# Kernel optimization log

Hardware: AMD Instinct MI355X
Metric: run time of the kernel (lower is better)

The kernel has to match this reference:

```python
import jax, jax.numpy as jnp
import numpy as np

EPS = 1e-5

def _conv(x, w, pad):
    return jax.lax.conv_general_dilated(
        x, w, window_strides=(1, 1), padding=((pad, pad), (pad, pad)),
        dimension_numbers=('NCHW', 'OIHW', 'NCHW'))

def _dyn_branch(x, w, d):
    # x: [N,C,H,W]; w: [N,9,H,W] softmax weights; d: dilation.
    # Equivalent to unfold(k=3, dilation=d, padding=d) + bmm with w,
    # done as 9 shifted zero-padded slices (row-major kernel order).
    N, C, H, W = x.shape
    xp = jnp.pad(x, ((0, 0), (0, 0), (d, d), (d, d)))
    out = jnp.zeros_like(x)
    k = 0
    for dy in (-d, 0, d):
        for dx in (-d, 0, d):
            patch = xp[:, :, d + dy:d + dy + H, d + dx:d + dx + W]
            out = out + patch * w[:, k:k + 1]
            k += 1
    return out

def setup_inputs() -> dict:
    key = jax.random.key(0)
    k1, k2, k3 = jax.random.split(key, 3)
    C = 256
    x = jax.random.normal(k1, (2, C, 96, 96), dtype=jnp.float32)
    W_cat = jax.random.normal(k2, (45, C, 3, 3), dtype=jnp.float32) * 0.05
    W_scale = jax.random.normal(k3, (C, 6 * C, 1, 1), dtype=jnp.float32) * 0.05
    gamma = jnp.ones((C,), dtype=jnp.float32)
    beta = jnp.zeros((C,), dtype=jnp.float32)
    return {"x": x, "W_cat": W_cat, "W_scale": W_scale, "gamma": gamma, "beta": beta}

def reference(x, W_cat, W_scale, gamma, beta):
    guidance = _conv(x, W_cat, pad=1)  # [N,45,H,W]
    outs = [x]
    for i, d in enumerate((1, 6, 12, 24, 36)):
        w = jax.nn.softmax(guidance[:, 9 * i:9 * (i + 1)], axis=1)  # [N,9,H,W]
        outs.append(_dyn_branch(x, w, d))
    cat = jnp.concatenate(outs, axis=1)  # [N, 6C, H, W]
    y = _conv(cat, W_scale, pad=0)       # [N, C, H, W]
    # BatchNorm2d in training mode (batch statistics, biased variance)
    mean = jnp.mean(y, axis=(0, 2, 3), keepdims=True)
    var = jnp.var(y, axis=(0, 2, 3), keepdims=True)
    y = (y - mean) * jax.lax.rsqrt(var + EPS)
    return y * gamma[None, :, None, None] + beta[None, :, None, None]
```

## Files before the change

### kernel.cpp

```cpp
#include <hip/hip_runtime.h>

typedef __bf16 bf16x8 __attribute__((ext_vector_type(8)));
typedef float f32x4 __attribute__((ext_vector_type(4)));

#define HW 9216
#define ZSLAB 9216
#define XTILE 32768

__device__ __forceinline__ unsigned short f2bf(float f) {
  unsigned u = __float_as_uint(f);
  unsigned r = (u + 0x7FFFu + ((u >> 16) & 1u)) >> 16;
  return (unsigned short)r;
}
__device__ __forceinline__ float bf2f(unsigned short h) {
  return __uint_as_float(((unsigned)h) << 16);
}

__device__ __forceinline__ void async16(const unsigned short* g, unsigned short* l) {
  __builtin_amdgcn_global_load_lds(
      (const __attribute__((address_space(1))) unsigned int*)g,
      (__attribute__((address_space(3))) unsigned int*)l, 16, 0, 0);
}

template <int O>
__device__ __forceinline__ void tapfma(float* y, uint4 lo, uint4 hi, uint4 wv) {
  const unsigned short* lu = (const unsigned short*)&lo;
  const unsigned short* hu = (const unsigned short*)&hi;
  const unsigned short* wu = (const unsigned short*)&wv;
#pragma unroll
  for (int j = 0; j < 8; ++j) {
    unsigned short zz = (O + j < 8) ? lu[O + j] : hu[O + j - 8];
    y[j] += bf2f(wu[j]) * bf2f(zz);
  }
}

__device__ __forceinline__ uint4 gload(const unsigned short* __restrict__ z,
                                       bool v, unsigned idx, unsigned guard) {
  return *(const uint4*)(z + (v ? idx : guard));
}

template <int B, int D>
__device__ __forceinline__ void branchU(float* y, const unsigned short* __restrict__ z,
                                        unsigned slab, unsigned guard,
                                        const unsigned short* __restrict__ gb,
                                        int h, int w0) {
  const bool cmv = ((unsigned)(w0 - ((D == 1 || D == 6) ? 8 : (D == 12 ? 16 : (D == 24 ? 24 : 40)))) <= 88u);
  const bool cm2v = ((unsigned)(w0 - ((D == 12) ? 8 : 32)) <= 88u);
  const bool cpv = ((unsigned)(w0 + ((D == 1 || D == 6) ? 8 : (D == 12 ? 16 : (D == 24 ? 24 : 40)))) <= 88u);
  const bool cp2v = ((unsigned)(w0 + ((D == 12) ? 8 : 32)) <= 88u);

#pragma unroll
  for (int r = 0; r < 3; ++r) {
    int hh = h + (r - 1) * D;
    bool rv = ((unsigned)hh < 96u);
    unsigned rb = slab + (unsigned)(hh * 96);
    const int K0 = (B - 1) * 9 + r * 3;
    uint4 wv0 = *(const uint4*)(gb + (size_t)((K0 + 0) * 2) * HW);
    uint4 wv1 = *(const uint4*)(gb + (size_t)((K0 + 1) * 2) * HW);
    uint4 wv2 = *(const uint4*)(gb + (size_t)((K0 + 2) * 2) * HW);
    if constexpr (D == 1 || D == 6) {
      uint4 Wm = gload(z, rv && cmv, rb + (unsigned)(w0 - 8), guard);
      uint4 W0 = gload(z, rv, rb + (unsigned)w0, guard);
      uint4 Wp = gload(z, rv && cpv, rb + (unsigned)(w0 + 8), guard);
      if constexpr (D == 1) {
        tapfma<7>(y, Wm, W0, wv0);
        tapfma<0>(y, W0, W0, wv1);
        tapfma<1>(y, W0, Wp, wv2);
      } else {
        tapfma<2>(y, Wm, W0, wv0);
        tapfma<0>(y, W0, W0, wv1);
        tapfma<6>(y, W0, Wp, wv2);
      }
    } else if constexpr (D == 24) {
      uint4 Wm = gload(z, rv && cmv, rb + (unsigned)(w0 - 24), guard);
      uint4 W0 = gload(z, rv, rb + (unsigned)w0, guard);
      uint4 Wp = gload(z, rv && cpv, rb + (unsigned)(w0 + 24), guard);
      tapfma<0>(y, Wm, Wm, wv0);
      tapfma<0>(y, W0, W0, wv1);
      tapfma<0>(y, Wp, Wp, wv2);
    } else {
      constexpr int co = (D == 12) ? 16 : 40;
      constexpr int ci = (D == 12) ? 8 : 32;
      uint4 Wa = gload(z, rv && cmv, rb + (unsigned)(w0 - co), guard);
      uint4 Wb = gload(z, rv && cm2v, rb + (unsigned)(w0 - ci), guard);
      uint4 W0 = gload(z, rv, rb + (unsigned)w0, guard);
      uint4 Wc = gload(z, rv && cp2v, rb + (unsigned)(w0 + ci), guard);
      uint4 Wd = gload(z, rv && cpv, rb + (unsigned)(w0 + co), guard);
      tapfma<4>(y, Wa, Wb, wv0);
      tapfma<0>(y, W0, W0, wv1);
      tapfma<4>(y, Wc, Wd, wv2);
    }
  }
}

__global__ __launch_bounds__(256) void init_all(const float* __restrict__ x,
                                                const float* __restrict__ Ws,
                                                const float* __restrict__ Wc,
                                                unsigned short* __restrict__ xb,
                                                unsigned short* __restrict__ Wsb,
                                                unsigned short* __restrict__ Wcb) {
  __shared__ float tile[64][65];
  int id = blockIdx.x;
  int t = threadIdx.x;
  if (id < 1152) {
    int bx = id % 144, by = (id / 144) % 4, n = id / 576;
    int p0 = bx * 64, ci0 = by * 64;
    int cl = t & 63, q = t >> 6;
#pragma unroll
    for (int i = 0; i < 16; ++i) {
      int cir = q + i * 4;
      tile[cir][cl] = x[((size_t)(n * 256 + ci0 + cir)) * HW + p0 + cl];
    }
    __syncthreads();
    int R = n * HW + p0 + cl;
    int Rt = R >> 7, Rl = R & 127;
#pragma unroll
    for (int i = 0; i < 2; ++i) {
      int cloc = q * 2 + i;
      unsigned rr[4];
#pragma unroll
      for (int jj = 0; jj < 4; ++jj) {
        unsigned short a = f2bf(tile[cloc * 8 + jj * 2][cl]);
        unsigned short b = f2bf(tile[cloc * 8 + jj * 2 + 1][cl]);
        rr[jj] = (unsigned)a | ((unsigned)b << 16);
      }
      *(uint4*)(xb + (size_t)Rt * XTILE + (by * 8 + cloc) * 1024 + Rl * 8) =
          make_uint4(rr[0], rr[1], rr[2], rr[3]);
    }
  } else {
    int u = (id - 1152) * 256 + t;
    if (u < 393216) {
      int r = u >> 8, k = u & 255;
      Wsb[(size_t)(r >> 7) * XTILE + (k >> 3) * 1024 + (r & 127) * 8 + (k & 7)] =
          f2bf(Ws[(size_t)(r & 255) * 1536 + (r >> 8) * 256 + k]);
    } else {
      int v = u - 393216;
      if (v < 110592) {
        int co = v / 2304, rr = v % 2304;
        int j = rr >> 8, ci = rr & 255;
        Wcb[v] = (co < 45) ? f2bf(Wc[(size_t)co * 2304 + ci * 9 + j]) : (unsigned short)0;
      }
    }
  }
}

__global__ __launch_bounds__(256) void gemms(const unsigned short* __restrict__ xb,
                                             const unsigned short* __restrict__ Wsb,
                                             const unsigned short* __restrict__ Wcb,
                                             unsigned short* __restrict__ z,
                                             unsigned short* __restrict__ gsmb) {
  __shared__ unsigned short smem[16384];
  int id = blockIdx.x;
  int t = threadIdx.x;
  int wid = t >> 6, lane = t & 63;
  int q = lane >> 4, ln = lane & 15;

  if (id < 288) {
    unsigned short* As = smem;
    unsigned short* Bs = smem + 4096;
    int m0 = id * 64;
    int mm = t >> 2, kq = t & 3;
    int m = m0 + mm;
    int img = m / HW, p = m % HW;
    int h = p / 96, w = p % 96;
    int mbase = img * HW;
    int nn = t >> 2;
    f32x4 acc[3] = {};
    uint4 aA0, aA1, aB0, aB1;

    {
      int hh = h - 1, ww = w - 1;
      bool valid = ((unsigned)hh < 96u) & ((unsigned)ww < 96u);
      int R = mbase + hh * 96 + ww;
      const unsigned short* pa =
          xb + (long)(R >> 7) * XTILE + kq * 1024 + (R & 127) * 8;
      aA0 = valid ? *(const uint4*)pa : make_uint4(0, 0, 0, 0);
      aA1 = valid ? *(const uint4*)(pa + 4096) : make_uint4(0, 0, 0, 0);
      if (t < 192) {
        const unsigned short* pb = Wcb + (size_t)nn * 2304 + kq * 8;
        aB0 = *(const uint4*)pb;
        aB1 = *(const uint4*)(pb + 32);
      }
    }

    for (int s = 0; s < 36; ++s) {
      ((uint4*)As)[kq * 64 + mm] = aA0;
      ((uint4*)As)[(kq + 4) * 64 + mm] = aA1;
      if (t < 192) {
        ((uint4*)Bs)[kq * 48 + nn] = aB0;
        ((uint4*)Bs)[(kq + 4) * 48 + nn] = aB1;
      }
      __syncthreads();
      if (s + 1 < 36) {
        int s1 = s + 1;
        int j = s1 >> 2;
        int hh = h + j / 3 - 1, ww = w + j % 3 - 1;
        bool valid = ((unsigned)hh < 96u) & ((unsigned)ww < 96u);
        int R = mbase + hh * 96 + ww;
        const unsigned short* pa = xb + (long)(R >> 7) * XTILE +
                                   ((s1 & 3) * 8 + kq) * 1024 + (R & 127) * 8;
        aA0 = valid ? *(const uint4*)pa : make_uint4(0, 0, 0, 0);
        aA1 = valid ? *(const uint4*)(pa + 4096) : make_uint4(0, 0, 0, 0);
        if (t < 192) {
          const unsigned short* pb = Wcb + (size_t)nn * 2304 + s1 * 64 + kq * 8;
          aB0 = *(const uint4*)pb;
          aB1 = *(const uint4*)(pb + 32);
        }
      }
#pragma unroll
      for (int kk = 0; kk < 2; ++kk) {
        bf16x8 a = ((const bf16x8*)As)[(kk * 4 + q) * 64 + wid * 16 + ln];
#pragma unroll
        for (int fn = 0; fn < 3; ++fn) {
          bf16x8 b = ((const bf16x8*)Bs)[(kk * 4 + q) * 48 + fn * 16 + ln];
          acc[fn] = __builtin_amdgcn_mfma_f32_16x16x32_bf16(a, b, acc[fn], 0, 0, 0);
        }
      }
      __syncthreads();
    }

    float* LDSf = (float*)smem;
#pragma unroll
    for (int fn = 0; fn < 3; ++fn)
#pragma unroll
      for (int r = 0; r < 4; ++r)
        LDSf[(wid * 16 + q * 4 + r) * 49 + fn * 16 + ln] = acc[fn][r];
    __syncthreads();
    if (t < 64) {
      const float* row = LDSf + t * 49;
      int mg = m0 + t;
      int img2 = mg / HW, p2 = mg - img2 * HW;
      for (int grp = 0; grp < 5; ++grp) {
        float v[9], mx = -1e30f;
#pragma unroll
        for (int k = 0; k < 9; ++k) { v[k] = row[grp * 9 + k]; mx = fmaxf(mx, v[k]); }
        float sum = 0.f;
#pragma unroll
        for (int k = 0; k < 9; ++k) { v[k] = __expf(v[k] - mx); sum += v[k]; }
        float inv = 1.f / sum;
#pragma unroll
        for (int k = 0; k < 9; ++k) {
          int col = grp * 9 + k;
          gsmb[((size_t)(col * 2 + img2)) * HW + p2] = f2bf(v[k] * inv);
        }
      }
    }
  } else {
    int zid = id - 288;
    int mt = zid % 144, ct = zid / 144;
    int m0 = mt * 128, c0 = ct * 128;
    int wm = (wid >> 1) * 64, wn = (wid & 1) * 64;
    bool isB = wid >= 2;
    const unsigned short* gsrc =
        (isB ? Wsb + (size_t)ct * XTILE : xb + (size_t)mt * XTILE) + lane * 8;
    unsigned short* lb = smem + (isB ? 8192 : 0);
    int ow = (wid & 1) * 4;
    f32x4 acc[4][4] = {};

#pragma unroll
    for (int kq = 0; kq < 4; ++kq)
      async16(gsrc + (ow + kq) * 512, lb + (ow + kq) * 512);
    __syncthreads();

    for (int s = 0; s < 8; ++s) {
      int cur = s & 1, nxt = cur ^ 1;
      if (s < 7) {
#pragma unroll
        for (int kq = 0; kq < 4; ++kq)
          async16(gsrc + (s + 1) * 4096 + (ow + kq) * 512,
                  lb + nxt * 4096 + (ow + kq) * 512);
      }
      const unsigned short* Asc = smem + cur * 4096;
      const unsigned short* Bsc = smem + 8192 + cur * 4096;
      bf16x8 a[4], b[4];
#pragma unroll
      for (int f = 0; f < 4; ++f) {
        a[f] = ((const bf16x8*)Asc)[q * 128 + wm + f * 16 + ln];
        b[f] = ((const bf16x8*)Bsc)[q * 128 + wn + f * 16 + ln];
      }
#pragma unroll
      for (int fm = 0; fm < 4; ++fm)
#pragma unroll
        for (int fn = 0; fn < 4; ++fn)
          acc[fm][fn] = __builtin_amdgcn_mfma_f32_16x16x32_bf16(a[fm], b[fn], acc[fm][fn], 0, 0, 0);
      __syncthreads();
    }

    int sl = c0 >> 8, cb = c0 & 255;
    int img = m0 / HW;
    int pbase = m0 - img * HW;
#pragma unroll
    for (int fm = 0; fm < 4; ++fm) {
      int p = pbase + wm + fm * 16 + q * 4;
#pragma unroll
      for (int fn = 0; fn < 4; ++fn) {
        int ch = cb + wn + fn * 16 + ln;
        size_t slab = ((size_t)(sl * 256 + ch) * 2 + img) * ZSLAB;
        unsigned lo = (unsigned)f2bf(acc[fm][fn][0]) | ((unsigned)f2bf(acc[fm][fn][1]) << 16);
        unsigned hi = (unsigned)f2bf(acc[fm][fn][2]) | ((unsigned)f2bf(acc[fm][fn][3]) << 16);
        *(uint2*)(z + slab + p) = make_uint2(lo, hi);
      }
    }
  }
}

__global__ __launch_bounds__(256) void accum_chw(const unsigned short* __restrict__ z,
                                                 const unsigned short* __restrict__ gsmb,
                                                 float* __restrict__ yacc,
                                                 float* __restrict__ stats,
                                                 unsigned guard) {
  int cid = blockIdx.x * 256 + threadIdx.x;
  int img = cid >= 294912;
  int rem = cid - img * 294912;
  int ch = rem / 1152;
  int pc = rem - ch * 1152;
  int h = pc / 12;
  int w0 = (pc - h * 12) * 8;
  int p0 = h * 96 + w0;

  unsigned chsl = (unsigned)(ch * 2 + img) * ZSLAB;
  const unsigned short* gb = gsmb + (size_t)img * HW + p0;

  float y[8];
  {
    uint4 v = *(const uint4*)(z + chsl + (unsigned)p0);
    const unsigned short* u = (const unsigned short*)&v;
#pragma unroll
    for (int j = 0; j < 8; ++j) y[j] = bf2f(u[j]);
  }
  branchU<1, 1>(y, z, chsl + 512u * ZSLAB, guard, gb, h, w0);
  branchU<2, 6>(y, z, chsl + 1024u * ZSLAB, guard, gb, h, w0);
  branchU<3, 12>(y, z, chsl + 1536u * ZSLAB, guard, gb, h, w0);
  branchU<4, 24>(y, z, chsl + 2048u * ZSLAB, guard, gb, h, w0);
  branchU<5, 36>(y, z, chsl + 2560u * ZSLAB, guard, gb, h, w0);

  size_t ybase = ((size_t)(img * 256 + ch)) * HW + p0;
  *(float4*)(yacc + ybase) = make_float4(y[0], y[1], y[2], y[3]);
  *(float4*)(yacc + ybase + 4) = make_float4(y[4], y[5], y[6], y[7]);

  float s1 = 0.f, s2 = 0.f;
#pragma unroll
  for (int j = 0; j < 8; ++j) { s1 += y[j]; s2 += y[j] * y[j]; }
#pragma unroll
  for (int off = 1; off <= 32; off <<= 1) {
    s1 += __shfl_xor(s1, off);
    s2 += __shfl_xor(s2, off);
  }
  if ((threadIdx.x & 63) == 0) {
    atomicAdd(&stats[ch], s1);
    atomicAdd(&stats[256 + ch], s2);
  }
}

__global__ __launch_bounds__(256) void bn_apply(const float* __restrict__ yacc,
                                                const float* __restrict__ stats,
                                                const float* __restrict__ gamma,
                                                const float* __restrict__ beta,
                                                float* __restrict__ out) {
  int q = blockIdx.x * 256 + threadIdx.x;
  int ch = (q / 2304) & 255;
  const float inv_cnt = 1.f / 18432.f;
  float mean = stats[ch] * inv_cnt;
  float var = stats[256 + ch] * inv_cnt - mean * mean;
  float sc = rsqrtf(var + 1e-5f) * gamma[ch];
  float sh = beta[ch] - mean * sc;
  float4 v = *(const float4*)(yacc + (size_t)q * 4);
  float4 o = make_float4(v.x * sc + sh, v.y * sc + sh, v.z * sc + sh, v.w * sc + sh);
  *(float4*)(out + (size_t)q * 4) = o;
}

extern "C" void kernel_launch(void* const* d_in, const int* in_sizes, int n_in,
                              void* d_out, int out_size, void* d_ws, size_t ws_size,
                              hipStream_t stream) {
  const float* x = (const float*)d_in[0];
  const float* Wc = (const float*)d_in[1];
  const float* Ws = (const float*)d_in[2];
  const float* gamma = (const float*)d_in[3];
  const float* beta = (const float*)d_in[4];
  float* out = (float*)d_out;

  unsigned short* xb = (unsigned short*)d_ws;
  unsigned short* Wsb = xb + 4718592;
  unsigned short* Wcb = Wsb + 393216;
  unsigned short* gsmb = Wcb + 110592;
  unsigned short* z = gsmb + 829440;
  float* yacc = (float*)(z + 28311552);
  float* stats = yacc + 4718592;
  const unsigned guard_idx = 28311552u + 9437184u + 1024u;

  hipMemsetAsync(stats, 0, 512 * sizeof(float) + 256, stream);
  init_all<<<3120, 256, 0, stream>>>(x, Ws, Wc, xb, Wsb, Wcb);
  gemms<<<2016, 256, 0, stream>>>(xb, Wsb, Wcb, z, gsmb);
  accum_chw<<<2304, 256, 0, stream>>>(z, gsmb, yacc, stats, guard_idx);
  bn_apply<<<4608, 256, 0, stream>>>(yacc, stats, gamma, beta, out);
}
```

Baseline: 202.8 us.

## Stage per-channel z slabs in LDS for dynamic-branch accumulation

The accumulation kernel now assigns one block per (channel, image) and uses async global-to-LDS copies to stage all six bf16 slabs (about 108KB) in shared memory. The shifted-tap reads then come from LDS instead of repeated global/L2 loads, with a zero guard entry in LDS handling out-of-range taps. The trade-off is one 576-thread block per CU at low occupancy and a serial copy-then-compute phase with no overlap between them.

```diff
diff --git a/kernel.cpp b/kernel.cpp
--- a/kernel.cpp
+++ b/kernel.cpp
@@ -6,6 +6,7 @@
 #define HW 9216
 #define ZSLAB 9216
 #define XTILE 32768
+#define GUARDL 55296
 
 __device__ __forceinline__ unsigned short f2bf(float f) {
   unsigned u = __float_as_uint(f);
@@ -34,16 +35,15 @@
   }
 }
 
-__device__ __forceinline__ uint4 gload(const unsigned short* __restrict__ z,
-                                       bool v, unsigned idx, unsigned guard) {
-  return *(const uint4*)(z + (v ? idx : guard));
+__device__ __forceinline__ uint4 lload(const unsigned short* lz, bool v, int idx) {
+  return *(const uint4*)(lz + (v ? idx : GUARDL));
 }
 
 template <int B, int D>
-__device__ __forceinline__ void branchU(float* y, const unsigned short* __restrict__ z,
-                                        unsigned slab, unsigned guard,
+__device__ __forceinline__ void branchL(float* y, const unsigned short* lz,
                                         const unsigned short* __restrict__ gb,
                                         int h, int w0) {
+  const int sbase = B * 9216;
   const bool cmv = ((unsigned)(w0 - ((D == 1 || D == 6) ? 8 : (D == 12 ? 16 : (D == 24 ? 24 : 40)))) <= 88u);
   const bool cm2v = ((unsigned)(w0 - ((D == 12) ? 8 : 32)) <= 88u);
   const bool cpv = ((unsigned)(w0 + ((D == 1 || D == 6) ? 8 : (D == 12 ? 16 : (D == 24 ? 24 : 40)))) <= 88u);
@@ -53,15 +53,15 @@
   for (int r = 0; r < 3; ++r) {
     int hh = h + (r - 1) * D;
     bool rv = ((unsigned)hh < 96u);
-    unsigned rb = slab + (unsigned)(hh * 96);
+    int rb = sbase + hh * 96;
     const int K0 = (B - 1) * 9 + r * 3;
     uint4 wv0 = *(const uint4*)(gb + (size_t)((K0 + 0) * 2) * HW);
     uint4 wv1 = *(const uint4*)(gb + (size_t)((K0 + 1) * 2) * HW);
     uint4 wv2 = *(const uint4*)(gb + (size_t)((K0 + 2) * 2) * HW);
     if constexpr (D == 1 || D == 6) {
-      uint4 Wm = gload(z, rv && cmv, rb + (unsigned)(w0 - 8), guard);
-      uint4 W0 = gload(z, rv, rb + (unsigned)w0, guard);
-      uint4 Wp = gload(z, rv && cpv, rb + (unsigned)(w0 + 8), guard);
+      uint4 Wm = lload(lz, rv && cmv, rb + w0 - 8);
+      uint4 W0 = lload(lz, rv, rb + w0);
+      uint4 Wp = lload(lz, rv && cpv, rb + w0 + 8);
       if constexpr (D == 1) {
         tapfma<7>(y, Wm, W0, wv0);
         tapfma<0>(y, W0, W0, wv1);
@@ -72,20 +72,20 @@
         tapfma<6>(y, W0, Wp, wv2);
       }
     } else if constexpr (D == 24) {
-      uint4 Wm = gload(z, rv && cmv, rb + (unsigned)(w0 - 24), guard);
-      uint4 W0 = gload(z, rv, rb + (unsigned)w0, guard);
-      uint4 Wp = gload(z, rv && cpv, rb + (unsigned)(w0 + 24), guard);
+      uint4 Wm = lload(lz, rv && cmv, rb + w0 - 24);
+      uint4 W0 = lload(lz, rv, rb + w0);
+      uint4 Wp = lload(lz, rv && cpv, rb + w0 + 24);
       tapfma<0>(y, Wm, Wm, wv0);
       tapfma<0>(y, W0, W0, wv1);
       tapfma<0>(y, Wp, Wp, wv2);
     } else {
       constexpr int co = (D == 12) ? 16 : 40;
       constexpr int ci = (D == 12) ? 8 : 32;
-      uint4 Wa = gload(z, rv && cmv, rb + (unsigned)(w0 - co), guard);
-      uint4 Wb = gload(z, rv && cm2v, rb + (unsigned)(w0 - ci), guard);
-      uint4 W0 = gload(z, rv, rb + (unsigned)w0, guard);
-      uint4 Wc = gload(z, rv && cp2v, rb + (unsigned)(w0 + ci), guard);
-      uint4 Wd = gload(z, rv && cpv, rb + (unsigned)(w0 + co), guard);
+      uint4 Wa = lload(lz, rv && cmv, rb + w0 - co);
+      uint4 Wb = lload(lz, rv && cm2v, rb + w0 - ci);
+      uint4 W0 = lload(lz, rv, rb + w0);
+      uint4 Wc = lload(lz, rv && cp2v, rb + w0 + ci);
+      uint4 Wd = lload(lz, rv && cpv, rb + w0 + co);
       tapfma<4>(y, Wa, Wb, wv0);
       tapfma<0>(y, W0, W0, wv1);
       tapfma<4>(y, Wc, Wd, wv2);
@@ -304,49 +304,63 @@
   }
 }
 
-__global__ __launch_bounds__(256) void accum_chw(const unsigned short* __restrict__ z,
-                                                 const unsigned short* __restrict__ gsmb,
-                                                 float* __restrict__ yacc,
-                                                 float* __restrict__ stats,
-                                                 unsigned guard) {
-  int cid = blockIdx.x * 256 + threadIdx.x;
-  int img = cid >= 294912;
-  int rem = cid - img * 294912;
-  int ch = rem / 1152;
-  int pc = rem - ch * 1152;
-  int h = pc / 12;
-  int w0 = (pc - h * 12) * 8;
-  int p0 = h * 96 + w0;
-
-  unsigned chsl = (unsigned)(ch * 2 + img) * ZSLAB;
-  const unsigned short* gb = gsmb + (size_t)img * HW + p0;
-
-  float y[8];
-  {
-    uint4 v = *(const uint4*)(z + chsl + (unsigned)p0);
-    const unsigned short* u = (const unsigned short*)&v;
-#pragma unroll
-    for (int j = 0; j < 8; ++j) y[j] = bf2f(u[j]);
-  }
-  branchU<1, 1>(y, z, chsl + 512u * ZSLAB, guard, gb, h, w0);
-  branchU<2, 6>(y, z, chsl + 1024u * ZSLAB, guard, gb, h, w0);
-  branchU<3, 12>(y, z, chsl + 1536u * ZSLAB, guard, gb, h, w0);
-  branchU<4, 24>(y, z, chsl + 2048u * ZSLAB, guard, gb, h, w0);
-  branchU<5, 36>(y, z, chsl + 2560u * ZSLAB, guard, gb, h, w0);
-
-  size_t ybase = ((size_t)(img * 256 + ch)) * HW + p0;
-  *(float4*)(yacc + ybase) = make_float4(y[0], y[1], y[2], y[3]);
-  *(float4*)(yacc + ybase + 4) = make_float4(y[4], y[5], y[6], y[7]);
+__global__ __launch_bounds__(576, 1) void accum_chw(const unsigned short* __restrict__ z,
+                                                    const unsigned short* __restrict__ gsmb,
+                                                    float* __restrict__ yacc,
+                                                    float* __restrict__ stats) {
+  extern __shared__ unsigned short lz[];
+  int bid = blockIdx.x;
+  int img = bid & 1, ch = bid >> 1;
+  int t = threadIdx.x;
+  int wv_id = t >> 6, lane = t & 63;
+
+#pragma unroll
+  for (int i = 0; i < 12; ++i) {
+    int op = wv_id + i * 9;
+    int s = op / 18;
+    int off = (op - s * 18) * 512;
+    async16(z + ((size_t)((s * 256 + ch) * 2 + img)) * ZSLAB + off + lane * 8,
+            lz + s * 9216 + off);
+  }
+  if (t == 0) *(uint4*)(lz + GUARDL) = make_uint4(0u, 0u, 0u, 0u);
+  __syncthreads();
 
   float s1 = 0.f, s2 = 0.f;
 #pragma unroll
-  for (int j = 0; j < 8; ++j) { s1 += y[j]; s2 += y[j] * y[j]; }
+  for (int rep = 0; rep < 2; ++rep) {
+    int c = t + rep * 576;
+    int h = c / 12;
+    int w0 = (c - h * 12) * 8;
+    int p0 = h * 96 + w0;
+    const unsigned short* gb = gsmb + (size_t)img * HW + p0;
+
+    float y[8];
+    {
+      uint4 v = *(const uint4*)(lz + p0);
+      const unsigned short* u = (const unsigned short*)&v;
+#pragma unroll
+      for (int j = 0; j < 8; ++j) y[j] = bf2f(u[j]);
+    }
+    branchL<1, 1>(y, lz, gb, h, w0);
+    branchL<2, 6>(y, lz, gb, h, w0);
+    branchL<3, 12>(y, lz, gb, h, w0);
+    branchL<4, 24>(y, lz, gb, h, w0);
+    branchL<5, 36>(y, lz, gb, h, w0);
+
+    size_t ybase = ((size_t)(img * 256 + ch)) * HW + p0;
+    *(float4*)(yacc + ybase) = make_float4(y[0], y[1], y[2], y[3]);
+    *(float4*)(yacc + ybase + 4) = make_float4(y[4], y[5], y[6], y[7]);
+
+#pragma unroll
+    for (int j = 0; j < 8; ++j) { s1 += y[j]; s2 += y[j] * y[j]; }
+  }
+
 #pragma unroll
   for (int off = 1; off <= 32; off <<= 1) {
     s1 += __shfl_xor(s1, off);
     s2 += __shfl_xor(s2, off);
   }
-  if ((threadIdx.x & 63) == 0) {
+  if (lane == 0) {
     atomicAdd(&stats[ch], s1);
     atomicAdd(&stats[256 + ch], s2);
   }
@@ -386,11 +400,10 @@
   unsigned short* z = gsmb + 829440;
   float* yacc = (float*)(z + 28311552);
   float* stats = yacc + 4718592;
-  const unsigned guard_idx = 28311552u + 9437184u + 1024u;
-
-  hipMemsetAsync(stats, 0, 512 * sizeof(float) + 256, stream);
+
+  hipMemsetAsync(stats, 0, 512 * sizeof(float), stream);
   init_all<<<3120, 256, 0, stream>>>(x, Ws, Wc, xb, Wsb, Wcb);
   gemms<<<2016, 256, 0, stream>>>(xb, Wsb, Wcb, z, gsmb);
-  accum_chw<<<2304, 256, 0, stream>>>(z, gsmb, yacc, stats, guard_idx);
+  accum_chw<<<512, 576, 110624, stream>>>(z, gsmb, yacc, stats);
   bn_apply<<<4608, 256, 0, stream>>>(yacc, stats, gamma, beta, out);
 }
```

New measurement: 173.5 us. 1.17x faster.
